# Kernel tuning notes

Measured on AMD Instinct MI355X. Metric: run time of the kernel, lower is better.

Reference implementation:

```python
import jax, jax.numpy as jnp
import numpy as np

B, L, D = 2, 2048, 1024
H = 16
HD = D // H            # 64
HALF = HD // 2         # 32
PHASE_SCALE = 1.0
SCALE = HD ** -0.5


def _orthogonal_projection(rng, d, m):
    g = rng.standard_normal((d, m)).astype(np.float32)
    q, r = np.linalg.qr(g)
    s = np.sign(np.diagonal(r))
    s = np.where(s == 0, 1.0, s).astype(np.float32)
    q = q * s[None, :]
    q = q * np.sqrt(d / m)  # preserve_variance=True
    return jnp.asarray(q)


def setup_inputs() -> dict:
    key = jax.random.key(0)
    ks = jax.random.split(key, 6)
    rng = np.random.default_rng(0)
    return {
        "x": jax.random.normal(ks[0], (B, L, D), dtype=jnp.float32),
        "p": jax.random.normal(ks[1], (B, L, D), dtype=jnp.float32),
        "Wqkv": jax.random.normal(ks[2], (D, 3 * D), dtype=jnp.float32) * (D ** -0.5),
        "bqkv": jax.random.normal(ks[3], (3 * D,), dtype=jnp.float32) * 0.02,
        "Wout": jax.random.normal(ks[4], (D, D), dtype=jnp.float32) * (D ** -0.5),
        "bout": jax.random.normal(ks[5], (D,), dtype=jnp.float32) * 0.02,
        "proj": _orthogonal_projection(rng, D, D // 2),
    }


def _rotate_half(t, cos, sin):
    # non-interleaved rotary: split head_dim in halves
    t1, t2 = t[..., :HALF], t[..., HALF:]
    return jnp.concatenate((t1 * cos - t2 * sin, t1 * sin + t2 * cos), axis=-1)


def reference(x, p, Wqkv, bqkv, Wout, bout, proj):
    Bx, Lx = x.shape[0], x.shape[1]
    # QKV projection -> (B, L, 3, H, HD)
    qkv = (x @ Wqkv + bqkv).reshape(Bx, Lx, 3, H, HD)
    q, k, v = qkv[:, :, 0], qkv[:, :, 1], qkv[:, :, 2]
    # collaborative rotary phases from conditioning tokens p
    phases = (p @ proj).reshape(Bx, Lx, H, HALF) * PHASE_SCALE
    cos, sin = jnp.cos(phases), jnp.sin(phases)
    q = _rotate_half(q, cos, sin)
    k = _rotate_half(k, cos, sin)
    # non-causal softmax attention, scale = head_dim^-0.5
    scores = jnp.einsum("blhd,bmhd->bhlm", q, k) * SCALE
    attn = jax.nn.softmax(scores, axis=-1)
    out = jnp.einsum("bhlm,bmhd->blhd", attn, v).reshape(Bx, Lx, D)
    return out @ Wout + bout
```

## Files before the change

### kernel.cpp

```cpp
#include <hip/hip_runtime.h>


typedef __bf16 bf16;
typedef __bf16 bf16x8 __attribute__((ext_vector_type(8)));
typedef __bf16 bf16x4 __attribute__((ext_vector_type(4)));
typedef float f32x4 __attribute__((ext_vector_type(4)));
typedef float f32x16 __attribute__((ext_vector_type(16)));
typedef unsigned int u32;

__device__ __forceinline__ bf16 f2bf(float f) {
  unsigned u = __builtin_bit_cast(unsigned, f);
  u += 0x7FFFu + ((u >> 16) & 1u);
  unsigned short h = (unsigned short)(u >> 16);
  return __builtin_bit_cast(bf16, h);
}

__device__ __forceinline__ void gload_lds16(const bf16* g, bf16* l) {
  __builtin_amdgcn_global_load_lds((const __attribute__((address_space(1))) u32*)(const void*)g,
                                   (__attribute__((address_space(3))) u32*)(void*)l, 16, 0, 0);
}

__device__ __forceinline__ u32 cvtpk_bf16(float lo, float hi) {
  u32 r;
  asm("v_cvt_pk_bf16_f32 %0, %1, %2" : "=v"(r) : "v"(lo), "v"(hi));
  return r;
}
__device__ __forceinline__ void perm32swap(u32& a, u32& b) {
  asm("v_permlane32_swap_b32 %0, %1" : "+v"(a), "+v"(b));
}

#if __has_builtin(__builtin_amdgcn_exp2f)
#define EXP2(x) __builtin_amdgcn_exp2f(x)
#else
#define EXP2(x) exp2f(x)
#endif

#define QSCALE 0.18033688f

__device__ __forceinline__ void xcd_remap(int& bx, int& by) {
  const int nx = gridDim.x;
  const int nwg = nx * gridDim.y;
  const int lin = blockIdx.y * nx + blockIdx.x;
  const int chunk = nwg >> 3;
  const int nid = (lin & 7) * chunk + (lin >> 3);
  bx = nid % nx;
  by = nid / nx;
}

__global__ __launch_bounds__(256) void k_prep(const float* __restrict__ x, bf16* __restrict__ xb,
                                              const float* __restrict__ p, bf16* __restrict__ pb,
                                              const float* __restrict__ W1, bf16* __restrict__ O1,
                                              const float* __restrict__ W2, bf16* __restrict__ O2,
                                              const float* __restrict__ W3, bf16* __restrict__ O3) {
  const int gb = blockIdx.x;
  if (gb < 8192) {
    int i = gb * 256 + threadIdx.x;
    const float* in = x; bf16* out = xb;
    if (i >= 1048576) { in = p; out = pb; i -= 1048576; }
    const float4 v = ((const float4*)in)[i];
    bf16x4 o;
    o[0] = f2bf(v.x); o[1] = f2bf(v.y); o[2] = f2bf(v.z); o[3] = f2bf(v.w);
    *(bf16x4*)(out + (size_t)i * 4) = o;
    return;
  }
  __shared__ float t[64][65];
  const int lin = gb - 8192;
  int bx = lin % 72;
  const int by = lin / 72;
  const float* in; bf16* out; int C;
  if (bx < 48)      { in = W1; out = O1; C = 3072; }
  else if (bx < 56) { in = W2; out = O2; C = 512;  bx -= 48; }
  else              { in = W3; out = O3; C = 1024; bx -= 56; }
  const int R = 1024;
  const int c0 = bx * 64, r0 = by * 64;
  for (int e = threadIdx.x; e < 4096; e += 256) {
    int r = e >> 6, c = e & 63;
    t[r][c] = in[(size_t)(r0 + r) * C + c0 + c];
  }
  __syncthreads();
  for (int e = threadIdx.x; e < 4096; e += 256) {
    int c = e >> 6, r = e & 63;
    out[(size_t)(c0 + c) * R + r0 + r] = f2bf(t[r][c]);
  }
}

__global__ __launch_bounds__(512, 2) void k_gemm128x8(const bf16* __restrict__ A,
                                                      const bf16* __restrict__ Bt,
                                                      const float* __restrict__ bias,
                                                      float* __restrict__ C,
                                                      int M, int N, int K) {
  __shared__ bf16 sA0[8192], sA1[8192];
  __shared__ bf16 sB0[8192], sB1[8192];
  const int tid = threadIdx.x;
  const int lane = tid & 63, w = tid >> 6;
  const int lrow = lane & 15, lgrp = lane >> 4;
  const int wm = (w >> 2) * 64, wn = (w & 3) * 32;
  int bx, by;
  xcd_remap(bx, by);
  const int m0 = bx * 128, n0 = by * 128;
  const int rsub = lane >> 3, slot = lane & 7;
  const int swz8 = (slot ^ rsub) * 8;
  const int r7 = lrow & 7;
  const int nkt = K >> 6;

  const bf16* Ab = A  + (size_t)m0 * K;
  const bf16* Bb = Bt + (size_t)n0 * K;

  f32x4 acc[4][2] = {};

#pragma unroll
  for (int c = 0; c < 2; ++c) {
    gload_lds16(Ab + (size_t)(c * 64 + w * 8 + rsub) * K + swz8, sA0 + c * 4096 + w * 512);
    gload_lds16(Bb + (size_t)(c * 64 + w * 8 + rsub) * K + swz8, sB0 + c * 4096 + w * 512);
  }
  __syncthreads();

  for (int kt = 0; kt < nkt; ++kt) {
    const bf16* pA = (kt & 1) ? sA1 : sA0;
    const bf16* pB = (kt & 1) ? sB1 : sB0;
    bf16* nA = (kt & 1) ? sA0 : sA1;
    bf16* nB = (kt & 1) ? sB0 : sB1;
    const size_t knext = (size_t)(kt + 1) * 64;
    const bool more = (kt < nkt - 1);

#pragma unroll
    for (int kk = 0; kk < 2; ++kk) {
      bf16x8 af[4], bfr[2];
#pragma unroll
      for (int mi = 0; mi < 4; ++mi)
        af[mi] = *(const bf16x8*)&pA[(wm + mi * 16 + lrow) * 64 + ((kk * 4 + lgrp) ^ r7) * 8];
#pragma unroll
      for (int ni = 0; ni < 2; ++ni)
        bfr[ni] = *(const bf16x8*)&pB[(wn + ni * 16 + lrow) * 64 + ((kk * 4 + lgrp) ^ r7) * 8];
      if (more) {
        const bf16* src = kk ? Bb : Ab;
        bf16* dst = kk ? nB : nA;
#pragma unroll
        for (int c = 0; c < 2; ++c)
          gload_lds16(src + (size_t)(c * 64 + w * 8 + rsub) * K + knext + swz8, dst + c * 4096 + w * 512);
      }
      __builtin_amdgcn_s_setprio(1);
#pragma unroll
      for (int mi = 0; mi < 4; ++mi)
#pragma unroll
        for (int ni = 0; ni < 2; ++ni)
          acc[mi][ni] = __builtin_amdgcn_mfma_f32_16x16x32_bf16(af[mi], bfr[ni], acc[mi][ni], 0, 0, 0);
      __builtin_amdgcn_s_setprio(0);
    }
    __syncthreads();
  }

#pragma unroll
  for (int mi = 0; mi < 4; ++mi)
#pragma unroll
    for (int ni = 0; ni < 2; ++ni) {
      const int col = n0 + wn + ni * 16 + lrow;
      const float bv = bias ? bias[col] : 0.f;
#pragma unroll
      for (int j = 0; j < 4; ++j) {
        const int row = m0 + wm + mi * 16 + lgrp * 4 + j;
        C[(size_t)row * N + col] = acc[mi][ni][j] + bv;
      }
    }
}

__global__ __launch_bounds__(256, 3) void k_gemm64(const bf16* __restrict__ A,
                                                   const bf16* __restrict__ Bt,
                                                   const float* __restrict__ bias,
                                                   float* __restrict__ C,
                                                   int M, int N, int K) {
  __shared__ bf16 sA0[4096], sA1[4096];
  __shared__ bf16 sB0[8192], sB1[8192];
  const int tid = threadIdx.x;
  const int lane = tid & 63, w = tid >> 6;
  const int lrow = lane & 15, lgrp = lane >> 4;
  const int wn = w * 32;
  int bx, by;
  xcd_remap(bx, by);
  const int m0 = bx * 64, n0 = by * 128;
  const int rsub = tid >> 3;
  const int swz8 = ((tid & 7) ^ (rsub & 7)) * 8;
  const int r7 = lrow & 7;
  const int nkt = K >> 6;

  const bf16* Ab = A  + (size_t)m0 * K;
  const bf16* Bb = Bt + (size_t)n0 * K;

  f32x4 acc[4][2] = {};

#pragma unroll
  for (int c = 0; c < 2; ++c)
    gload_lds16(Ab + (size_t)(c * 32 + rsub) * K + swz8, sA0 + c * 2048 + w * 512);
#pragma unroll
  for (int c = 0; c < 4; ++c)
    gload_lds16(Bb + (size_t)(c * 32 + rsub) * K + swz8, sB0 + c * 2048 + w * 512);
  __syncthreads();

  for (int kt = 0; kt < nkt; ++kt) {
    const bf16* pA = (kt & 1) ? sA1 : sA0;
    const bf16* pB = (kt & 1) ? sB1 : sB0;
    bf16* nA = (kt & 1) ? sA0 : sA1;
    bf16* nB = (kt & 1) ? sB0 : sB1;
    const size_t knext = (size_t)(kt + 1) * 64;
    const bool more = (kt < nkt - 1);

#pragma unroll
    for (int kk = 0; kk < 2; ++kk) {
      bf16x8 af[4], bfr[2];
#pragma unroll
      for (int mi = 0; mi < 4; ++mi)
        af[mi] = *(const bf16x8*)&pA[(mi * 16 + lrow) * 64 + ((kk * 4 + lgrp) ^ r7) * 8];
#pragma unroll
      for (int ni = 0; ni < 2; ++ni)
        bfr[ni] = *(const bf16x8*)&pB[(wn + ni * 16 + lrow) * 64 + ((kk * 4 + lgrp) ^ r7) * 8];
      if (more) {
        if (kk == 0) {
#pragma unroll
          for (int c = 0; c < 2; ++c)
            gload_lds16(Ab + (size_t)(c * 32 + rsub) * K + knext + swz8, nA + c * 2048 + w * 512);
        } else {
#pragma unroll
          for (int c = 0; c < 4; ++c)
            gload_lds16(Bb + (size_t)(c * 32 + rsub) * K + knext + swz8, nB + c * 2048 + w * 512);
        }
      }
      __builtin_amdgcn_s_setprio(1);
#pragma unroll
      for (int mi = 0; mi < 4; ++mi)
#pragma unroll
        for (int ni = 0; ni < 2; ++ni)
          acc[mi][ni] = __builtin_amdgcn_mfma_f32_16x16x32_bf16(af[mi], bfr[ni], acc[mi][ni], 0, 0, 0);
      __builtin_amdgcn_s_setprio(0);
    }
    __syncthreads();
  }

#pragma unroll
  for (int mi = 0; mi < 4; ++mi)
#pragma unroll
    for (int ni = 0; ni < 2; ++ni) {
      const int col = n0 + wn + ni * 16 + lrow;
      const float bv = bias ? bias[col] : 0.f;
#pragma unroll
      for (int j = 0; j < 4; ++j) {
        const int row = m0 + mi * 16 + lgrp * 4 + j;
        C[(size_t)row * N + col] = acc[mi][ni][j] + bv;
      }
    }
}

__global__ __launch_bounds__(512, 2) void k_gemm_qkv256(const bf16* __restrict__ A,
                                                        const bf16* __restrict__ Bt,
                                                        const float* __restrict__ bqkv,
                                                        const float* __restrict__ phases,
                                                        bf16* __restrict__ qb,
                                                        bf16* __restrict__ kb,
                                                        bf16* __restrict__ vb) {
  __shared__ bf16 sA0[16384], sA1[16384];
  __shared__ bf16 sB0[16384], sB1[16384];
  const int tid = threadIdx.x;
  const int lane = tid & 63, w = tid >> 6;
  const int lrow = lane & 15, lgrp = lane >> 4;
  const int wm = (w >> 2) * 128;
  const int wn = (w & 3) * 64;
  const int m0 = blockIdx.x * 256, n0 = blockIdx.y * 256;
  const int K = 1024;

  const int srow = tid >> 3;
  const int swz8 = (((tid & 7) ^ (srow & 7))) * 8;
  const int r7 = lrow & 7;

  const bf16* Ab = A  + (size_t)m0 * K;
  const bf16* Bb = Bt + (size_t)n0 * K;

  f32x4 acc[8][4] = {};

#pragma unroll
  for (int g = 0; g < 4; ++g) {
    gload_lds16(Ab + (size_t)(g * 64 + srow) * K + swz8, sA0 + g * 4096 + w * 512);
    gload_lds16(Bb + (size_t)(g * 64 + srow) * K + swz8, sB0 + g * 4096 + w * 512);
  }
  __syncthreads();

  for (int kt = 0; kt < 16; ++kt) {
    const bf16* pA = (kt & 1) ? sA1 : sA0;
    const bf16* pB = (kt & 1) ? sB1 : sB0;
    bf16* nA = (kt & 1) ? sA0 : sA1;
    bf16* nB = (kt & 1) ? sB0 : sB1;
    const size_t knext = (size_t)(kt + 1) * 64;

    bf16x8 bfr[4][2];
#pragma unroll
    for (int ni = 0; ni < 4; ++ni)
#pragma unroll
      for (int kk = 0; kk < 2; ++kk)
        bfr[ni][kk] = *(const bf16x8*)&pB[(wn + ni * 16 + lrow) * 64 + ((kk * 4 + lgrp) ^ r7) * 8];

#pragma unroll
    for (int q = 0; q < 4; ++q) {
      if (kt < 15) {
        gload_lds16(Ab + (size_t)(q * 64 + srow) * K + knext + swz8, nA + q * 4096 + w * 512);
        gload_lds16(Bb + (size_t)(q * 64 + srow) * K + knext + swz8, nB + q * 4096 + w * 512);
      }
      bf16x8 af[2][2];
#pragma unroll
      for (int m2 = 0; m2 < 2; ++m2)
#pragma unroll
        for (int kk = 0; kk < 2; ++kk)
          af[m2][kk] = *(const bf16x8*)&pA[(wm + (q * 2 + m2) * 16 + lrow) * 64 + ((kk * 4 + lgrp) ^ r7) * 8];
      __builtin_amdgcn_s_setprio(1);
#pragma unroll
      for (int m2 = 0; m2 < 2; ++m2)
#pragma unroll
        for (int ni = 0; ni < 4; ++ni)
#pragma unroll
          for (int kk = 0; kk < 2; ++kk)
            acc[q * 2 + m2][ni] =
                __builtin_amdgcn_mfma_f32_16x16x32_bf16(af[m2][kk], bfr[ni][kk], acc[q * 2 + m2][ni], 0, 0, 0);
      __builtin_amdgcn_s_setprio(0);
    }
    __syncthreads();
  }

  const int nw = n0 + wn;
  const int sec = nw >> 10;
  const int hh = (nw & 1023) >> 6;
  const float b0 = bqkv[nw + lrow];
  const float b1 = bqkv[nw + 16 + lrow];
  const float b2 = bqkv[nw + 32 + lrow];
  const float b3 = bqkv[nw + 48 + lrow];

  if (sec == 2) {
#pragma unroll
    for (int mi = 0; mi < 8; ++mi) {
      const int row0 = m0 + wm + mi * 16 + lgrp * 4;
      const int b = row0 >> 11, l0 = row0 & 2047;
#pragma unroll
      for (int ni = 0; ni < 4; ++ni) {
        const int d = ni * 16 + lrow;
        const float bv = (ni == 0) ? b0 : (ni == 1) ? b1 : (ni == 2) ? b2 : b3;
        bf16x4 pv;
#pragma unroll
        for (int j = 0; j < 4; ++j) pv[j] = f2bf(acc[mi][ni][j] + bv);
        *(bf16x4*)&vb[(((size_t)(b * 16 + hh)) * 64 + d) * 2048 + l0] = pv;
      }
    }
  } else {
    bf16* qk = sec ? kb : qb;
    const float qs = sec ? 1.0f : QSCALE;
#pragma unroll
    for (int mi = 0; mi < 8; ++mi) {
#pragma unroll
      for (int j = 0; j < 4; ++j) {
        const int row = m0 + wm + mi * 16 + lgrp * 4 + j;
        const int b = row >> 11, l = row & 2047;
        const float ph1 = phases[(size_t)row * 512 + hh * 32 + lrow];
        const float ph2 = phases[(size_t)row * 512 + hh * 32 + 16 + lrow];
        float s1, c1, s2, c2;
        __sincosf(ph1, &s1, &c1);
        __sincosf(ph2, &s2, &c2);
        const float t0 = acc[mi][0][j] + b0;
        const float t1 = acc[mi][1][j] + b1;
        const float t2 = acc[mi][2][j] + b2;
        const float t3 = acc[mi][3][j] + b3;
        bf16* base = qk + (((size_t)(b * 16 + hh)) * 2048 + l) * 64;
        base[lrow]      = f2bf((t0 * c1 - t2 * s1) * qs);
        base[16 + lrow] = f2bf((t1 * c2 - t3 * s2) * qs);
        base[32 + lrow] = f2bf((t0 * s1 + t2 * c1) * qs);
        base[48 + lrow] = f2bf((t1 * s2 + t3 * c2) * qs);
      }
    }
  }
}

__global__ __launch_bounds__(256, 4) void k_flash_attn8(const bf16* __restrict__ qb,
                                                        const bf16* __restrict__ kb,
                                                        const bf16* __restrict__ vb,
                                                        bf16* __restrict__ attnout) {
  const int tid = threadIdx.x, lane = tid & 63, w = tid >> 6;
  const int ql = lane & 31, hi = lane >> 5;
  const int tsel = w >> 1;
  const int qh = w & 1;
  const int fid = blockIdx.x;
  const int nid = (fid & 7) * 128 + (fid >> 3);
  const int qblk = nid & 31, h = (nid >> 5) & 15, b = nid >> 9;
  const size_t bh = (size_t)b * 16 + h;
  const bf16* Kp = kb + bh * 2048 * 64;
  const bf16* Vp = vb + bh * 64 * 2048;

  __shared__ __align__(16) char smem[32768];
  bf16* sK = (bf16*)smem;
  bf16* sV = (bf16*)(smem + 16384);

  const bf16* Qp = qb + (bh * 2048 + (size_t)qblk * 64 + qh * 32 + ql) * 64;
  bf16x8 qf[4];
#pragma unroll
  for (int c = 0; c < 4; ++c) qf[c] = *(const bf16x8*)(Qp + c * 16 + hi * 8);

  const int srow = tid >> 3;
  const int swz = (tid & 7) ^ (srow & 7);
  const int jv0 = (tsel * 4 + 0 + hi) ^ (ql & 7);
  const int jv1 = (tsel * 4 + 2 + hi) ^ (ql & 7);

  f32x16 o0 = {}, o1 = {};
  float lsum = 0.f;
  u32 pcu[8];
  bf16x8 vfr[4];

#define STAGE(BUF, KV0)                                                                       \
  do {                                                                                        \
    gload_lds16(Kp + (size_t)((KV0) + srow) * 64 + swz * 8,        sK + (BUF) * 4096 + w * 512); \
    gload_lds16(Kp + (size_t)((KV0) + srow + 32) * 64 + swz * 8,   sK + (BUF) * 4096 + 2048 + w * 512); \
    gload_lds16(Vp + (size_t)srow * 2048 + (KV0) + swz * 8,        sV + (BUF) * 4096 + w * 512); \
    gload_lds16(Vp + (size_t)(srow + 32) * 2048 + (KV0) + swz * 8, sV + (BUF) * 4096 + 2048 + w * 512); \
  } while (0)

#define SM_PACK(CUR)                                                                \
  do {                                                                              \
    const bf16* sVc = sV + (CUR) * 4096;                                            \
    _Pragma("unroll")                                                               \
    for (int j2 = 0; j2 < 16; ++j2) {                                               \
      float pv = EXP2(st0[j2]);                                                     \
      st0[j2] = pv; lsum += pv;                                                     \
    }                                                                               \
    {                                                                               \
      u32 a0 = cvtpk_bf16(st0[0], st0[1]),  a1 = cvtpk_bf16(st0[2], st0[3]);        \
      u32 a2 = cvtpk_bf16(st0[4], st0[5]),  a3 = cvtpk_bf16(st0[6], st0[7]);        \
      perm32swap(a0, a2); perm32swap(a1, a3);                                       \
      pcu[0] = a0; pcu[1] = a1; pcu[2] = a2; pcu[3] = a3;                           \
      u32 b0 = cvtpk_bf16(st0[8], st0[9]),  b1 = cvtpk_bf16(st0[10], st0[11]);      \
      u32 b2 = cvtpk_bf16(st0[12], st0[13]), b3 = cvtpk_bf16(st0[14], st0[15]);     \
      perm32swap(b0, b2); perm32swap(b1, b3);                                       \
      pcu[4] = b0; pcu[5] = b1; pcu[6] = b2; pcu[7] = b3;                           \
    }                                                                               \
    vfr[0] = *(const bf16x8*)&sVc[ql * 64 + jv0 * 8];                               \
    vfr[1] = *(const bf16x8*)&sVc[(32 + ql) * 64 + jv0 * 8];                        \
    vfr[2] = *(const bf16x8*)&sVc[ql * 64 + jv1 * 8];                               \
    vfr[3] = *(const bf16x8*)&sVc[(32 + ql) * 64 + jv1 * 8];                        \
  } while (0)

#define PV_PREV()                                                                   \
  do {                                                                              \
    union { u32 u[4]; bf16x8 v; } cA, cB;                                           \
    cA.u[0] = pcu[0]; cA.u[1] = pcu[1]; cA.u[2] = pcu[2]; cA.u[3] = pcu[3];         \
    cB.u[0] = pcu[4]; cB.u[1] = pcu[5]; cB.u[2] = pcu[6]; cB.u[3] = pcu[7];         \
    __builtin_amdgcn_s_setprio(1);                                                  \
    o0 = __builtin_amdgcn_mfma_f32_32x32x16_bf16(vfr[0], cA.v, o0, 0, 0, 0);        \
    o1 = __builtin_amdgcn_mfma_f32_32x32x16_bf16(vfr[1], cA.v, o1, 0, 0, 0);        \
    o0 = __builtin_amdgcn_mfma_f32_32x32x16_bf16(vfr[2], cB.v, o0, 0, 0, 0);        \
    o1 = __builtin_amdgcn_mfma_f32_32x32x16_bf16(vfr[3], cB.v, o1, 0, 0, 0);        \
    __builtin_amdgcn_s_setprio(0);                                                  \
  } while (0)

  STAGE(0, 0);
  __syncthreads();

  {
    const bf16* sKc = sK;
    f32x16 st0 = {};
#pragma unroll
    for (int c = 0; c < 4; ++c) {
      const int j = (c * 2 + hi) ^ (ql & 7);
      bf16x8 kf = *(const bf16x8*)&sKc[(tsel * 32 + ql) * 64 + j * 8];
      __builtin_amdgcn_s_setprio(1);
      st0 = __builtin_amdgcn_mfma_f32_32x32x16_bf16(kf, qf[c], st0, 0, 0, 0);
      __builtin_amdgcn_s_setprio(0);
    }
    STAGE(1, 64);
    SM_PACK(0);
    __syncthreads();
  }

  for (int t = 1; t < 32; ++t) {
    const int cur = t & 1;
    const bf16* sKc = sK + cur * 4096;

    f32x16 st0 = {};
#pragma unroll
    for (int c = 0; c < 4; ++c) {
      const int j = (c * 2 + hi) ^ (ql & 7);
      bf16x8 kf = *(const bf16x8*)&sKc[(tsel * 32 + ql) * 64 + j * 8];
      __builtin_amdgcn_s_setprio(1);
      st0 = __builtin_amdgcn_mfma_f32_32x32x16_bf16(kf, qf[c], st0, 0, 0, 0);
      __builtin_amdgcn_s_setprio(0);
    }
    PV_PREV();
    if (t < 31) STAGE(cur ^ 1, (t + 1) * 64);
    SM_PACK(cur);
    __syncthreads();
  }

  PV_PREV();

  float* cb = (float*)smem;
  if (w >= 2) {
    const int idx = ((w - 2) * 64 + lane) * 34;
#pragma unroll
    for (int i = 0; i < 16; ++i) cb[idx + i] = o0[i];
#pragma unroll
    for (int i = 0; i < 16; ++i) cb[idx + 16 + i] = o1[i];
    cb[idx + 32] = lsum;
  }
  __syncthreads();
  if (w < 2) {
    const int idx = (w * 64 + lane) * 34;
#pragma unroll
    for (int i = 0; i < 16; ++i) o0[i] += cb[idx + i];
#pragma unroll
    for (int i = 0; i < 16; ++i) o1[i] += cb[idx + 16 + i];
    lsum += cb[idx + 32];
    lsum += __shfl_xor(lsum, 32);

    const float inv = 1.f / lsum;
    const int qrow = qblk * 64 + qh * 32 + ql;
    bf16* outp = attnout + ((size_t)b * 2048 + qrow) * 1024 + h * 64;
#pragma unroll
    for (int j2 = 0; j2 < 4; ++j2) {
      bf16x4 ov;
#pragma unroll
      for (int jj = 0; jj < 4; ++jj) ov[jj] = f2bf(o0[j2 * 4 + jj] * inv);
      *(bf16x4*)(outp + j2 * 8 + hi * 4) = ov;
#pragma unroll
      for (int jj = 0; jj < 4; ++jj) ov[jj] = f2bf(o1[j2 * 4 + jj] * inv);
      *(bf16x4*)(outp + 32 + j2 * 8 + hi * 4) = ov;
    }
  }
#undef STAGE
#undef SM_PACK
#undef PV_PREV
}

extern "C" void kernel_launch(void* const* d_in, const int* in_sizes, int n_in,
                              void* d_out, int out_size, void* d_ws, size_t ws_size,
                              hipStream_t stream) {
  (void)in_sizes; (void)n_in; (void)out_size; (void)ws_size;
  const float* x    = (const float*)d_in[0];
  const float* p    = (const float*)d_in[1];
  const float* Wqkv = (const float*)d_in[2];
  const float* bqkv = (const float*)d_in[3];
  const float* Wout = (const float*)d_in[4];
  const float* bout = (const float*)d_in[5];
  const float* proj = (const float*)d_in[6];
  float* out = (float*)d_out;

  char* ws = (char*)d_ws;
  size_t off = 0;
  bf16* xb     = (bf16*)(ws + off); off += (size_t)4096 * 1024 * 2;
  bf16* pb     = (bf16*)(ws + off); off += (size_t)4096 * 1024 * 2;
  bf16* WqkvT  = (bf16*)(ws + off); off += (size_t)3072 * 1024 * 2;
  bf16* projT  = (bf16*)(ws + off); off += (size_t)512  * 1024 * 2;
  bf16* WoutT  = (bf16*)(ws + off); off += (size_t)1024 * 1024 * 2;
  float* phases= (float*)(ws + off); off += (size_t)4096 * 512 * 4;
  bf16* qb     = (bf16*)(ws + off); off += (size_t)4096 * 1024 * 2;
  bf16* kb     = (bf16*)(ws + off); off += (size_t)4096 * 1024 * 2;
  bf16* vb     = (bf16*)(ws + off); off += (size_t)4096 * 1024 * 2;
  bf16* attnb  = (bf16*)(ws + off); off += (size_t)4096 * 1024 * 2;

  k_prep<<<9344, 256, 0, stream>>>(x, xb, p, pb, Wqkv, WqkvT, proj, projT, Wout, WoutT);

  k_gemm64<<<dim3(64, 4), 256, 0, stream>>>(pb, projT, nullptr, phases, 4096, 512, 1024);
  k_gemm_qkv256<<<dim3(16, 12), 512, 0, stream>>>(xb, WqkvT, bqkv, phases, qb, kb, vb);

  k_flash_attn8<<<1024, 256, 0, stream>>>(qb, kb, vb, attnb);

  k_gemm128x8<<<dim3(32, 8), 512, 0, stream>>>(attnb, WoutT, bout, out, 4096, 1024, 1024);
}
```

Measured before the change: 132.3 us.

## Shrink QKV GEMM tile to 128x128 with XCD-aware block remapping

The fused QKV+rotary GEMM changes from 256x256 tiles (192 blocks) to 128x128 tiles (768 blocks), with a new 8-warp layout of 32x64 per warp and an XCD remap of block indices. Prefetch loads are now split per k-substep, A during one and B during the other. The goal is to fill all CUs of the MI355X, since 192 blocks underfill 256 CUs, and to improve L2 locality per XCD. In exchange each tile reuses less data and makes more global and LDS traffic per FLOP.

```diff
diff --git a/kernel.cpp b/kernel.cpp
--- a/kernel.cpp
+++ b/kernel.cpp
@@ -249,36 +249,37 @@
     }
 }
 
-__global__ __launch_bounds__(512, 2) void k_gemm_qkv256(const bf16* __restrict__ A,
+__global__ __launch_bounds__(512, 2) void k_gemm_qkv128(const bf16* __restrict__ A,
                                                         const bf16* __restrict__ Bt,
                                                         const float* __restrict__ bqkv,
                                                         const float* __restrict__ phases,
                                                         bf16* __restrict__ qb,
                                                         bf16* __restrict__ kb,
                                                         bf16* __restrict__ vb) {
-  __shared__ bf16 sA0[16384], sA1[16384];
-  __shared__ bf16 sB0[16384], sB1[16384];
+  __shared__ bf16 sA0[8192], sA1[8192];
+  __shared__ bf16 sB0[8192], sB1[8192];
   const int tid = threadIdx.x;
   const int lane = tid & 63, w = tid >> 6;
   const int lrow = lane & 15, lgrp = lane >> 4;
-  const int wm = (w >> 2) * 128;
-  const int wn = (w & 3) * 64;
-  const int m0 = blockIdx.x * 256, n0 = blockIdx.y * 256;
+  const int wm = (w >> 1) * 32;
+  const int wn = (w & 1) * 64;
+  int bx, by;
+  xcd_remap(bx, by);
+  const int m0 = bx * 128, n0 = by * 128;
+  const int rsub = lane >> 3, slot = lane & 7;
+  const int swz8 = (slot ^ rsub) * 8;
+  const int r7 = lrow & 7;
   const int K = 1024;
-
-  const int srow = tid >> 3;
-  const int swz8 = (((tid & 7) ^ (srow & 7))) * 8;
-  const int r7 = lrow & 7;
 
   const bf16* Ab = A  + (size_t)m0 * K;
   const bf16* Bb = Bt + (size_t)n0 * K;
 
-  f32x4 acc[8][4] = {};
-
-#pragma unroll
-  for (int g = 0; g < 4; ++g) {
-    gload_lds16(Ab + (size_t)(g * 64 + srow) * K + swz8, sA0 + g * 4096 + w * 512);
-    gload_lds16(Bb + (size_t)(g * 64 + srow) * K + swz8, sB0 + g * 4096 + w * 512);
+  f32x4 acc[2][4] = {};
+
+#pragma unroll
+  for (int c = 0; c < 2; ++c) {
+    gload_lds16(Ab + (size_t)(c * 64 + w * 8 + rsub) * K + swz8, sA0 + c * 4096 + w * 512);
+    gload_lds16(Bb + (size_t)(c * 64 + w * 8 + rsub) * K + swz8, sB0 + c * 4096 + w * 512);
   }
   __syncthreads();
 
@@ -288,35 +289,30 @@
     bf16* nA = (kt & 1) ? sA0 : sA1;
     bf16* nB = (kt & 1) ? sB0 : sB1;
     const size_t knext = (size_t)(kt + 1) * 64;
-
-    bf16x8 bfr[4][2];
-#pragma unroll
-    for (int ni = 0; ni < 4; ++ni)
-#pragma unroll
-      for (int kk = 0; kk < 2; ++kk)
-        bfr[ni][kk] = *(const bf16x8*)&pB[(wn + ni * 16 + lrow) * 64 + ((kk * 4 + lgrp) ^ r7) * 8];
-
-#pragma unroll
-    for (int q = 0; q < 4; ++q) {
-      if (kt < 15) {
-        gload_lds16(Ab + (size_t)(q * 64 + srow) * K + knext + swz8, nA + q * 4096 + w * 512);
-        gload_lds16(Bb + (size_t)(q * 64 + srow) * K + knext + swz8, nB + q * 4096 + w * 512);
-      }
-      bf16x8 af[2][2];
-#pragma unroll
-      for (int m2 = 0; m2 < 2; ++m2)
-#pragma unroll
-        for (int kk = 0; kk < 2; ++kk)
-          af[m2][kk] = *(const bf16x8*)&pA[(wm + (q * 2 + m2) * 16 + lrow) * 64 + ((kk * 4 + lgrp) ^ r7) * 8];
+    const bool more = (kt < 15);
+
+#pragma unroll
+    for (int kk = 0; kk < 2; ++kk) {
+      bf16x8 af[2], bfr[4];
+#pragma unroll
+      for (int mi = 0; mi < 2; ++mi)
+        af[mi] = *(const bf16x8*)&pA[(wm + mi * 16 + lrow) * 64 + ((kk * 4 + lgrp) ^ r7) * 8];
+#pragma unroll
+      for (int ni = 0; ni < 4; ++ni)
+        bfr[ni] = *(const bf16x8*)&pB[(wn + ni * 16 + lrow) * 64 + ((kk * 4 + lgrp) ^ r7) * 8];
+      if (more) {
+        const bf16* src = kk ? Bb : Ab;
+        bf16* dst = kk ? nB : nA;
+#pragma unroll
+        for (int c = 0; c < 2; ++c)
+          gload_lds16(src + (size_t)(c * 64 + w * 8 + rsub) * K + knext + swz8, dst + c * 4096 + w * 512);
+      }
       __builtin_amdgcn_s_setprio(1);
 #pragma unroll
-      for (int m2 = 0; m2 < 2; ++m2)
+      for (int mi = 0; mi < 2; ++mi)
 #pragma unroll
         for (int ni = 0; ni < 4; ++ni)
-#pragma unroll
-          for (int kk = 0; kk < 2; ++kk)
-            acc[q * 2 + m2][ni] =
-                __builtin_amdgcn_mfma_f32_16x16x32_bf16(af[m2][kk], bfr[ni][kk], acc[q * 2 + m2][ni], 0, 0, 0);
+          acc[mi][ni] = __builtin_amdgcn_mfma_f32_16x16x32_bf16(af[mi], bfr[ni], acc[mi][ni], 0, 0, 0);
       __builtin_amdgcn_s_setprio(0);
     }
     __syncthreads();
@@ -332,7 +328,7 @@
 
   if (sec == 2) {
 #pragma unroll
-    for (int mi = 0; mi < 8; ++mi) {
+    for (int mi = 0; mi < 2; ++mi) {
       const int row0 = m0 + wm + mi * 16 + lgrp * 4;
       const int b = row0 >> 11, l0 = row0 & 2047;
 #pragma unroll
@@ -349,7 +345,7 @@
     bf16* qk = sec ? kb : qb;
     const float qs = sec ? 1.0f : QSCALE;
 #pragma unroll
-    for (int mi = 0; mi < 8; ++mi) {
+    for (int mi = 0; mi < 2; ++mi) {
 #pragma unroll
       for (int j = 0; j < 4; ++j) {
         const int row = m0 + wm + mi * 16 + lgrp * 4 + j;
@@ -559,7 +555,7 @@
   k_prep<<<9344, 256, 0, stream>>>(x, xb, p, pb, Wqkv, WqkvT, proj, projT, Wout, WoutT);
 
   k_gemm64<<<dim3(64, 4), 256, 0, stream>>>(pb, projT, nullptr, phases, 4096, 512, 1024);
-  k_gemm_qkv256<<<dim3(16, 12), 512, 0, stream>>>(xb, WqkvT, bqkv, phases, qb, kb, vb);
+  k_gemm_qkv128<<<dim3(32, 24), 512, 0, stream>>>(xb, WqkvT, bqkv, phases, qb, kb, vb);
 
   k_flash_attn8<<<1024, 256, 0, stream>>>(qb, kb, vb, attnb);
 
```

New measurement: 134.7 us. No clear change (+1.8%).
